# Kernel tuning notes

Measured on AMD Instinct MI355X. Metric: run time of the kernel, lower is better.

## Reference

```python
import jax, jax.numpy as jnp
import numpy as np
import math

D = 1024
H = 16
HEAD_D = D // H  # 64
T = 2048
B = 4


def setup_inputs() -> dict:
    key = jax.random.key(0)
    k1, k2, k3 = jax.random.split(key, 3)
    x = jax.random.normal(k1, (B, T, D), dtype=jnp.float32)
    # c_attn: Linear(d, d + 2*head_d, bias=False) -> weight applied as x @ W
    w_attn = jax.random.normal(k2, (D, D + 2 * HEAD_D), dtype=jnp.float32) * (1.0 / math.sqrt(D))
    w_proj = jax.random.normal(k3, (D, D), dtype=jnp.float32) * (1.0 / math.sqrt(D))
    return {"x": x, "w_attn": w_attn, "w_proj": w_proj}


def reference(x, w_attn, w_proj):
    Bv, Tv, _ = x.shape
    qkv = x @ w_attn  # [B,T,D+2*head_d]
    q = qkv[..., :D].reshape(Bv, Tv, H, HEAD_D).transpose(0, 2, 1, 3)  # [B,H,T,hd]
    k = qkv[..., D:D + HEAD_D]        # [B,T,hd] single shared KV head
    v = qkv[..., D + HEAD_D:]         # [B,T,hd]
    scale = 1.0 / math.sqrt(HEAD_D)
    # att: [B,H,T,T], shared K broadcast over H query heads
    att = jnp.einsum('bhqd,bkd->bhqk', q, k) * scale
    causal = jnp.tril(jnp.ones((Tv, Tv), dtype=bool))  # [T,T]
    att = jnp.where(causal[None, None, :, :], att, -jnp.inf)
    att = jax.nn.softmax(att, axis=-1)
    y = jnp.einsum('bhqk,bkd->bhqd', att, v)           # [B,H,T,hd]
    y = y.transpose(0, 2, 1, 3).reshape(Bv, Tv, D)     # [B,T,D]
    return y @ w_proj
```

## Files before the change

kernel.cpp:

```cpp
#include <hip/hip_runtime.h>

typedef unsigned short u16;
typedef unsigned int u32;
typedef __attribute__((ext_vector_type(8))) short short8;
typedef __attribute__((ext_vector_type(4))) float f32x4;
typedef __attribute__((ext_vector_type(4))) u16 u16x4;

__device__ __forceinline__ u16 f2bf(float f) {
  union { float f; unsigned u; } x; x.f = f;
  unsigned r = (x.u + 0x7fffu + ((x.u >> 16) & 1u)) >> 16;
  return (u16)r;
}

__device__ __forceinline__ u16 f2bf_rna(float f) {
  union { float f; u32 u; } x; x.f = f;
  return (u16)((x.u + 0x8000u) >> 16);
}

__device__ __forceinline__ f32x4 mfma16(short8 a, short8 b, f32x4 c) {
  return __builtin_amdgcn_mfma_f32_16x16x32_bf16(a, b, c, 0, 0, 0);
}

__device__ __forceinline__ void gload16(const u16* g, u16* l) {
  __builtin_amdgcn_global_load_lds((const __attribute__((address_space(1))) void*)g,
                                   (__attribute__((address_space(3))) void*)l, 16, 0, 0);
}

__global__ __launch_bounds__(256) void prep(const float* __restrict__ x,
                                            const float* __restrict__ w_attn,
                                            const float* __restrict__ w_proj,
                                            u16* __restrict__ xb,
                                            u16* __restrict__ wat,
                                            u16* __restrict__ wpt) {
  __shared__ float tile[32][33];
  const int bid = blockIdx.x, tid = threadIdx.x;
  if (bid >= 2176) {
    const int id = bid - 2176;
    const f32x4* src = (const f32x4*)(x + (size_t)id * 4096);
    u16x4* dst = (u16x4*)(xb + (size_t)id * 4096);
#pragma unroll
    for (int c = 0; c < 4; ++c) {
      f32x4 v = src[c * 256 + tid];
      u16x4 o;
#pragma unroll
      for (int j = 0; j < 4; ++j) o[j] = f2bf(v[j]);
      dst[c * 256 + tid] = o;
    }
    return;
  }
  const float* src; u16* dst; int C, bx, by;
  if (bid < 1152) { src = w_attn; dst = wat; C = 1152; bx = bid % 36; by = bid / 36; }
  else { int id = bid - 1152; src = w_proj; dst = wpt; C = 1024; bx = id & 31; by = id >> 5; }
  const int R = 1024;
  const int tx = tid & 31, ty = tid >> 5;
  int c = bx * 32 + tx, r0 = by * 32;
#pragma unroll
  for (int i = 0; i < 32; i += 8)
    tile[ty + i][tx] = src[(size_t)(r0 + ty + i) * C + c];
  __syncthreads();
  int oc = r0 + tx, orow0 = bx * 32;
#pragma unroll
  for (int i = 0; i < 32; i += 8)
    dst[(size_t)(orow0 + ty + i) * R + oc] = f2bf(tile[tx][ty + i]);
}

template <bool C_F32, bool VT>
__global__ __launch_bounds__(256) void gemm_bt(const u16* __restrict__ A,
                                               const u16* __restrict__ Bt,
                                               void* __restrict__ Cp,
                                               u16* __restrict__ vt,
                                               int lda, int ldb, int ldc, int K) {
  __shared__ u16 As[128 * 32];
  __shared__ u16 Bs[128 * 32];
  const int tid = threadIdx.x;
  const int wid = tid >> 6, lane = tid & 63;
  const int quad = lane >> 4, l15 = lane & 15;
  const int m0 = blockIdx.y * 128, n0 = blockIdx.x * 128;
  const int wm = (wid & 1) * 64, wn = (wid >> 1) * 64;
  const int sr = tid >> 2;
  const int sc = (tid & 3) * 8;

  f32x4 acc[4][4] = {};

  for (int k0 = 0; k0 < K; k0 += 32) {
    __syncthreads();
#pragma unroll
    for (int cch = 0; cch < 2; ++cch) {
      int row = sr + cch * 64;
      gload16(A + (size_t)(m0 + row) * lda + k0 + sc, &As[wid * 512 + cch * 2048]);
      gload16(Bt + (size_t)(n0 + row) * ldb + k0 + sc, &Bs[wid * 512 + cch * 2048]);
    }
    __syncthreads();
    short8 a[4], b[4];
#pragma unroll
    for (int i = 0; i < 4; ++i) a[i] = *(const short8*)&As[(wm + 16 * i + l15) * 32 + quad * 8];
#pragma unroll
    for (int j = 0; j < 4; ++j) b[j] = *(const short8*)&Bs[(wn + 16 * j + l15) * 32 + quad * 8];
#pragma unroll
    for (int i = 0; i < 4; ++i)
#pragma unroll
      for (int j = 0; j < 4; ++j)
        acc[i][j] = mfma16(a[i], b[j], acc[i][j]);
  }

#pragma unroll
  for (int i = 0; i < 4; ++i) {
#pragma unroll
    for (int j = 0; j < 4; ++j) {
      const int mrow = m0 + wm + 16 * i + quad * 4;
      const int ncol = n0 + wn + 16 * j + l15;
#pragma unroll
      for (int r = 0; r < 4; ++r) {
        float v = acc[i][j][r];
        if (C_F32) {
          ((float*)Cp)[(size_t)(mrow + r) * ldc + ncol] = v;
        } else {
          u16 hv = f2bf(v);
          ((u16*)Cp)[(size_t)(mrow + r) * ldc + ncol] = hv;
          if (VT) {
            if (ncol >= 1088) {
              int mg = mrow + r;
              int bb = mg >> 11, tt = mg & 2047;
              vt[(size_t)(bb * 64 + (ncol - 1088)) * 2048 + tt] = hv;
            }
          }
        }
      }
    }
  }
}

__global__ __launch_bounds__(256) void attn_kernel(const u16* __restrict__ qkv,
                                                   const u16* __restrict__ vt,
                                                   u16* __restrict__ y) {
  const int T = 2048, LD = 1152;
  __shared__ u16 Ks[64 * 72];
  __shared__ u16 Vts[64 * 72];
  __shared__ u16 Pw[4][2][16 * 72];

  const int bid = blockIdx.x;
  const int qt = 15 - (bid >> 6);
  const int bh = bid & 63, b = bh >> 4, h = bh & 15;
  const int q0 = qt * 128;
  const int tid = threadIdx.x, wid = tid >> 6, lane = tid & 63;
  const int quad = lane >> 4, l15 = lane & 15;
  const int wq = wid * 32;
  const u16* qkvb = qkv + (size_t)b * T * LD;
  const u16* vtb = vt + (size_t)b * 64 * 2048;
  const int sr0 = (tid * 8) >> 6, sc0 = (tid * 8) & 63;
  const int sr1 = sr0 + 32;
  const float c1 = 0.18033688f;
  const float M = 18.0f;
  short8 ones;
#pragma unroll
  for (int j = 0; j < 8; ++j) ones[j] = (short)0x3F80;

  short8 qreg[2][2];
#pragma unroll
  for (int jt = 0; jt < 2; ++jt)
#pragma unroll
    for (int ks = 0; ks < 2; ++ks)
      qreg[jt][ks] = *(const short8*)(qkvb + (size_t)(q0 + wq + 16 * jt + l15) * LD + h * 64 + ks * 32 + quad * 8);

  f32x4 acc[4][2] = {};
  f32x4 accs[2] = {};

  short8 kr0 = *(const short8*)(qkvb + (size_t)sr0 * LD + 1024 + sc0);
  short8 kr1 = *(const short8*)(qkvb + (size_t)sr1 * LD + 1024 + sc0);
  short8 vr0 = *(const short8*)(vtb + (size_t)sr0 * 2048 + sc0);
  short8 vr1 = *(const short8*)(vtb + (size_t)sr1 * 2048 + sc0);

  const int ktmax = 2 * qt + 2;
  for (int kt = 0; kt < ktmax; ++kt) {
    const int kv0 = kt * 64;
    __syncthreads();
    *(short8*)&Ks[sr0 * 72 + sc0] = kr0;
    *(short8*)&Ks[sr1 * 72 + sc0] = kr1;
    *(short8*)&Vts[sr0 * 72 + sc0] = vr0;
    *(short8*)&Vts[sr1 * 72 + sc0] = vr1;
    __syncthreads();
    if (kt + 1 < ktmax) {
      const int nv0 = kv0 + 64;
      kr0 = *(const short8*)(qkvb + (size_t)(nv0 + sr0) * LD + 1024 + sc0);
      kr1 = *(const short8*)(qkvb + (size_t)(nv0 + sr1) * LD + 1024 + sc0);
      vr0 = *(const short8*)(vtb + (size_t)sr0 * 2048 + nv0 + sc0);
      vr1 = *(const short8*)(vtb + (size_t)sr1 * 2048 + nv0 + sc0);
    }
    if (kv0 > q0 + wq + 31) continue;

    f32x4 st[4][2] = {};
#pragma unroll
    for (int ks = 0; ks < 2; ++ks) {
      short8 kf[4];
#pragma unroll
      for (int i = 0; i < 4; ++i) kf[i] = *(const short8*)&Ks[(16 * i + l15) * 72 + ks * 32 + quad * 8];
#pragma unroll
      for (int i = 0; i < 4; ++i)
#pragma unroll
        for (int jt = 0; jt < 2; ++jt)
          st[i][jt] = mfma16(kf[i], qreg[jt][ks], st[i][jt]);
    }

    const bool needMask = (kv0 + 63 > q0 + wq);
#pragma unroll
    for (int jt = 0; jt < 2; ++jt) {
      u16* pw = &Pw[wid][jt][0];
      const int qg = q0 + wq + 16 * jt + l15;
#pragma unroll
      for (int i = 0; i < 4; ++i) {
        u16x4 pk;
#pragma unroll
        for (int r = 0; r < 4; ++r) {
          float p = __builtin_amdgcn_exp2f(fmaf(st[i][jt][r], c1, -M));
          if (needMask && (kv0 + 16 * i + quad * 4 + r > qg)) p = 0.f;
          pk[r] = f2bf_rna(p);
        }
        *(u16x4*)&pw[l15 * 72 + 16 * i + quad * 4] = pk;
      }
    }

#pragma unroll
    for (int ks = 0; ks < 2; ++ks) {
      short8 pf[2];
#pragma unroll
      for (int jt = 0; jt < 2; ++jt)
        pf[jt] = *(const short8*)&Pw[wid][jt][l15 * 72 + ks * 32 + quad * 8];
#pragma unroll
      for (int id = 0; id < 4; ++id) {
        short8 vf = *(const short8*)&Vts[(16 * id + l15) * 72 + ks * 32 + quad * 8];
        acc[id][0] = mfma16(vf, pf[0], acc[id][0]);
        acc[id][1] = mfma16(vf, pf[1], acc[id][1]);
      }
      accs[0] = mfma16(ones, pf[0], accs[0]);
      accs[1] = mfma16(ones, pf[1], accs[1]);
    }
  }

#pragma unroll
  for (int jt = 0; jt < 2; ++jt) {
    const float inv = 1.f / accs[jt][0];
    const int qg = q0 + wq + 16 * jt + l15;
#pragma unroll
    for (int id = 0; id < 4; ++id) {
      u16x4 o;
#pragma unroll
      for (int r = 0; r < 4; ++r) o[r] = f2bf(acc[id][jt][r] * inv);
      *(u16x4*)(y + (size_t)(b * T + qg) * 1024 + h * 64 + 16 * id + quad * 4) = o;
    }
  }
}

extern "C" void kernel_launch(void* const* d_in, const int* in_sizes, int n_in,
                              void* d_out, int out_size, void* d_ws, size_t ws_size,
                              hipStream_t stream) {
  const float* x = (const float*)d_in[0];
  const float* w_attn = (const float*)d_in[1];
  const float* w_proj = (const float*)d_in[2];
  float* out = (float*)d_out;
  char* ws = (char*)d_ws;

  u16* wat = (u16*)ws;
  u16* wpt = (u16*)(ws + 2359296);
  u16* xb  = (u16*)(ws + 4456448);
  u16* qkv = (u16*)(ws + 21233664);
  u16* vt  = (u16*)(ws + 40108032);
  u16* y   = (u16*)(ws + 41156608);

  prep<<<dim3(4224), dim3(256), 0, stream>>>(x, w_attn, w_proj, xb, wat, wpt);
  gemm_bt<false, true><<<dim3(9, 64), 256, 0, stream>>>(xb, wat, qkv, vt, 1024, 1024, 1152, 1024);
  attn_kernel<<<dim3(1024), dim3(256), 0, stream>>>(qkv, vt, y);
  gemm_bt<true, false><<<dim3(8, 64), 256, 0, stream>>>(y, wpt, out, nullptr, 1024, 1024, 1024, 1024);
}
```

Before: 220.5 us.

## Double-buffer GEMM LDS tiles and shrink attention LDS padding and P buffer

```diff
diff --git a/kernel.cpp b/kernel.cpp
--- a/kernel.cpp
+++ b/kernel.cpp
@@ -70,8 +70,8 @@
                                                void* __restrict__ Cp,
                                                u16* __restrict__ vt,
                                                int lda, int ldb, int ldc, int K) {
-  __shared__ u16 As[128 * 32];
-  __shared__ u16 Bs[128 * 32];
+  __shared__ u16 As[2][128 * 32];
+  __shared__ u16 Bs[2][128 * 32];
   const int tid = threadIdx.x;
   const int wid = tid >> 6, lane = tid & 63;
   const int quad = lane >> 4, l15 = lane & 15;
@@ -82,20 +82,27 @@
 
   f32x4 acc[4][4] = {};
 
-  for (int k0 = 0; k0 < K; k0 += 32) {
+  auto stage = [&](int t, int bb) {
+    const int k0 = t << 5;
+#pragma unroll
+    for (int cch = 0; cch < 2; ++cch) {
+      const int row = sr + cch * 64;
+      gload16(A + (size_t)(m0 + row) * lda + k0 + sc, &As[bb][wid * 512 + cch * 2048]);
+      gload16(Bt + (size_t)(n0 + row) * ldb + k0 + sc, &Bs[bb][wid * 512 + cch * 2048]);
+    }
+  };
+
+  const int nk = K >> 5;
+  stage(0, 0);
+  for (int t = 0; t < nk; ++t) {
+    const int bb = t & 1;
     __syncthreads();
-#pragma unroll
-    for (int cch = 0; cch < 2; ++cch) {
-      int row = sr + cch * 64;
-      gload16(A + (size_t)(m0 + row) * lda + k0 + sc, &As[wid * 512 + cch * 2048]);
-      gload16(Bt + (size_t)(n0 + row) * ldb + k0 + sc, &Bs[wid * 512 + cch * 2048]);
-    }
-    __syncthreads();
+    if (t + 1 < nk) stage(t + 1, bb ^ 1);
     short8 a[4], b[4];
 #pragma unroll
-    for (int i = 0; i < 4; ++i) a[i] = *(const short8*)&As[(wm + 16 * i + l15) * 32 + quad * 8];
-#pragma unroll
-    for (int j = 0; j < 4; ++j) b[j] = *(const short8*)&Bs[(wn + 16 * j + l15) * 32 + quad * 8];
+    for (int i = 0; i < 4; ++i) a[i] = *(const short8*)&As[bb][(wm + 16 * i + l15) * 32 + quad * 8];
+#pragma unroll
+    for (int j = 0; j < 4; ++j) b[j] = *(const short8*)&Bs[bb][(wn + 16 * j + l15) * 32 + quad * 8];
 #pragma unroll
     for (int i = 0; i < 4; ++i)
 #pragma unroll
@@ -120,8 +127,8 @@
           if (VT) {
             if (ncol >= 1088) {
               int mg = mrow + r;
-              int bb = mg >> 11, tt = mg & 2047;
-              vt[(size_t)(bb * 64 + (ncol - 1088)) * 2048 + tt] = hv;
+              int bb2 = mg >> 11, tt = mg & 2047;
+              vt[(size_t)(bb2 * 64 + (ncol - 1088)) * 2048 + tt] = hv;
             }
           }
         }
@@ -134,9 +141,9 @@
                                                    const u16* __restrict__ vt,
                                                    u16* __restrict__ y) {
   const int T = 2048, LD = 1152;
-  __shared__ u16 Ks[64 * 72];
-  __shared__ u16 Vts[64 * 72];
-  __shared__ u16 Pw[4][2][16 * 72];
+  __shared__ u16 Ks[64 * 68];
+  __shared__ u16 Vts[64 * 68];
+  __shared__ u16 Pw[4][16 * 68];
 
   const int bid = blockIdx.x;
   const int qt = 15 - (bid >> 6);
@@ -147,7 +154,7 @@
   const int wq = wid * 32;
   const u16* qkvb = qkv + (size_t)b * T * LD;
   const u16* vtb = vt + (size_t)b * 64 * 2048;
-  const int sr0 = (tid * 8) >> 6, sc0 = (tid * 8) & 63;
+  const int sr0 = tid >> 3, sc0 = (tid & 7) * 8;
   const int sr1 = sr0 + 32;
   const float c1 = 0.18033688f;
   const float M = 18.0f;
@@ -174,10 +181,10 @@
   for (int kt = 0; kt < ktmax; ++kt) {
     const int kv0 = kt * 64;
     __syncthreads();
-    *(short8*)&Ks[sr0 * 72 + sc0] = kr0;
-    *(short8*)&Ks[sr1 * 72 + sc0] = kr1;
-    *(short8*)&Vts[sr0 * 72 + sc0] = vr0;
-    *(short8*)&Vts[sr1 * 72 + sc0] = vr1;
+    *(short8*)&Ks[sr0 * 68 + sc0] = kr0;
+    *(short8*)&Ks[sr1 * 68 + sc0] = kr1;
+    *(short8*)&Vts[sr0 * 68 + sc0] = vr0;
+    *(short8*)&Vts[sr1 * 68 + sc0] = vr1;
     __syncthreads();
     if (kt + 1 < ktmax) {
       const int nv0 = kv0 + 64;
@@ -193,7 +200,7 @@
     for (int ks = 0; ks < 2; ++ks) {
       short8 kf[4];
 #pragma unroll
-      for (int i = 0; i < 4; ++i) kf[i] = *(const short8*)&Ks[(16 * i + l15) * 72 + ks * 32 + quad * 8];
+      for (int i = 0; i < 4; ++i) kf[i] = *(const short8*)&Ks[(16 * i + l15) * 68 + ks * 32 + quad * 8];
 #pragma unroll
       for (int i = 0; i < 4; ++i)
 #pragma unroll
@@ -202,9 +209,9 @@
     }
 
     const bool needMask = (kv0 + 63 > q0 + wq);
+    u16* pw = Pw[wid];
 #pragma unroll
     for (int jt = 0; jt < 2; ++jt) {
-      u16* pw = &Pw[wid][jt][0];
       const int qg = q0 + wq + 16 * jt + l15;
 #pragma unroll
       for (int i = 0; i < 4; ++i) {
@@ -215,24 +222,18 @@
           if (needMask && (kv0 + 16 * i + quad * 4 + r > qg)) p = 0.f;
           pk[r] = f2bf_rna(p);
         }
-        *(u16x4*)&pw[l15 * 72 + 16 * i + quad * 4] = pk;
+        *(u16x4*)&pw[l15 * 68 + 16 * i + quad * 4] = pk;
       }
-    }
-
-#pragma unroll
-    for (int ks = 0; ks < 2; ++ks) {
-      short8 pf[2];
-#pragma unroll
-      for (int jt = 0; jt < 2; ++jt)
-        pf[jt] = *(const short8*)&Pw[wid][jt][l15 * 72 + ks * 32 + quad * 8];
-#pragma unroll
-      for (int id = 0; id < 4; ++id) {
-        short8 vf = *(const short8*)&Vts[(16 * id + l15) * 72 + ks * 32 + quad * 8];
-        acc[id][0] = mfma16(vf, pf[0], acc[id][0]);
-        acc[id][1] = mfma16(vf, pf[1], acc[id][1]);
+#pragma unroll
+      for (int ks = 0; ks < 2; ++ks) {
+        short8 pf = *(const short8*)&pw[l15 * 68 + ks * 32 + quad * 8];
+#pragma unroll
+        for (int id = 0; id < 4; ++id) {
+          short8 vf = *(const short8*)&Vts[(16 * id + l15) * 68 + ks * 32 + quad * 8];
+          acc[id][jt] = mfma16(vf, pf, acc[id][jt]);
+        }
+        accs[jt] = mfma16(ones, pf, accs[jt]);
       }
-      accs[0] = mfma16(ones, pf[0], accs[0]);
-      accs[1] = mfma16(ones, pf[1], accs[1]);
     }
   }
 
```

New measurement: 250.8 us. 1.14x slower.
